# Kernel tuning notes

Measured on AMD Instinct MI355X. Metric: run time of the kernel, lower is better.

## Reference

```python
import jax, jax.numpy as jnp
import numpy as np

B, S = 128, 32
V, E, H, L = 32000, 512, 1024, 2


def setup_inputs() -> dict:
    key = jax.random.key(0)
    ks = jax.random.split(key, 16)
    s = 0.02  # weight scale
    inp = {
        "x": jax.random.randint(ks[0], (B, S), 0, V),
        "encoder_output": jax.random.normal(ks[1], (S, B, H), jnp.float32),  # unused by module
        "encoder_hidden_state": jax.random.normal(ks[2], (L, B, H), jnp.float32),
        "emb": jax.random.normal(ks[3], (V, E), jnp.float32) * s,
        "w_ih0": jax.random.normal(ks[4], (3 * H, E), jnp.float32) * s,
        "w_hh0": jax.random.normal(ks[5], (3 * H, H), jnp.float32) * s,
        "b_ih0": jax.random.normal(ks[6], (3 * H,), jnp.float32) * s,
        "b_hh0": jax.random.normal(ks[7], (3 * H,), jnp.float32) * s,
        "w_ih1": jax.random.normal(ks[8], (3 * H, H), jnp.float32) * s,
        "w_hh1": jax.random.normal(ks[9], (3 * H, H), jnp.float32) * s,
        "b_ih1": jax.random.normal(ks[10], (3 * H,), jnp.float32) * s,
        "b_hh1": jax.random.normal(ks[11], (3 * H,), jnp.float32) * s,
        "w_dec": jax.random.normal(ks[12], (V, H), jnp.float32) * s,
        "b_dec": jax.random.normal(ks[13], (V,), jnp.float32) * s,
        "max_seq_length": S,
    }
    return inp


def _gru_cell(h, xt, w_ih, w_hh, b_ih, b_hh):
    # PyTorch GRU gate math
    gi = xt @ w_ih.T + b_ih  # [B, 3H]
    gh = h @ w_hh.T + b_hh   # [B, 3H]
    ir, iz, inn = jnp.split(gi, 3, axis=-1)
    hr, hz, hn = jnp.split(gh, 3, axis=-1)
    r = jax.nn.sigmoid(ir + hr)
    z = jax.nn.sigmoid(iz + hz)
    n = jnp.tanh(inn + r * hn)
    return (1.0 - z) * n + z * h


def reference(x, encoder_output, encoder_hidden_state, emb,
              w_ih0, w_hh0, b_ih0, b_hh0,
              w_ih1, w_hh1, b_ih1, b_hh1,
              w_dec, b_dec, max_seq_length):
    # teaching_rate = 0.0 -> pure teacher forcing; dropout p=0.0 -> identity.
    # Step 0 consumes SOS token (id 1, from torch.ones().long()); steps 1..T-1 consume x[:, i].
    Bsz = x.shape[0]
    sos = jnp.ones((Bsz, 1), jnp.int32)
    toks = jnp.concatenate([sos, x[:, 1:max_seq_length].astype(jnp.int32)], axis=1)  # [B, T]
    xs = emb[toks].transpose(1, 0, 2)  # [T, B, E] (seq-first, matching permute(1,0,2))

    def step(carry, xt):
        h0, h1 = carry
        h0 = _gru_cell(h0, xt, w_ih0, w_hh0, b_ih0, b_hh0)
        h1 = _gru_cell(h1, h0, w_ih1, w_hh1, b_ih1, b_hh1)
        return (h0, h1), h1

    init = (encoder_hidden_state[0], encoder_hidden_state[1])
    _, ys = jax.lax.scan(step, init, xs)  # ys: [T, B, H]
    logits = jnp.einsum('tbh,vh->tbv', ys, w_dec) + b_dec  # [T, B, V]
    return logits
```

## Files before the change

### kernel.cpp

```cpp
#include <hip/hip_runtime.h>
#include <hip/hip_bf16.h>
#include <stdint.h>

#define T_SEQ 32
#define BATCH 128
#define EMB   512
#define HID   1024
#define VOC   32000
#define G3    (3 * HID)
#define MROWS (T_SEQ * BATCH)
#define BHID  (BATCH * HID)

typedef __bf16 bf16_t;
typedef __bf16 bf16x8 __attribute__((ext_vector_type(8)));
typedef __bf16 bf16x4 __attribute__((ext_vector_type(4)));
typedef float  f32x4  __attribute__((ext_vector_type(4)));

#define MFMA(a, b, c) __builtin_amdgcn_mfma_f32_16x16x32_bf16((a), (b), (c), 0, 0, 0)

__global__ void f32_to_bf16_kernel(const float* __restrict__ in,
                                   bf16_t* __restrict__ out, int n) {
    int i = (blockIdx.x * blockDim.x + threadIdx.x) * 4;
    if (i + 3 < n) {
        float4 v = *(const float4*)(in + i);
        out[i + 0] = (bf16_t)v.x;
        out[i + 1] = (bf16_t)v.y;
        out[i + 2] = (bf16_t)v.z;
        out[i + 3] = (bf16_t)v.w;
    } else {
        for (; i < n; ++i) out[i] = (bf16_t)in[i];
    }
}

__global__ void embed_kernel(const int* __restrict__ x,
                             const float* __restrict__ emb,
                             bf16_t* __restrict__ X) {
    int m = blockIdx.x;
    int t = m >> 7, b = m & 127;
    int tok = (t == 0) ? 1 : x[b * T_SEQ + t];
    const float* src = emb + (size_t)tok * EMB;
    bf16_t* dst = X + (size_t)m * EMB;
    int c = threadIdx.x * 4;
    float4 v = *(const float4*)(src + c);
    dst[c + 0] = (bf16_t)v.x;
    dst[c + 1] = (bf16_t)v.y;
    dst[c + 2] = (bf16_t)v.z;
    dst[c + 3] = (bf16_t)v.w;
}

#define GLOAD_LDS16(g, l)                                                    \
    __builtin_amdgcn_global_load_lds(                                        \
        (const __attribute__((address_space(1))) void*)(g),                  \
        (__attribute__((address_space(3))) void*)(l), 16, 0, 0)

template <int BIAS>
__global__ __launch_bounds__(256) void gemm_bf16_kernel(
    const bf16_t* __restrict__ A, const bf16_t* __restrict__ B,
    const float* __restrict__ bias, float* __restrict__ C,
    int M, int N, int K) {
    __shared__ __align__(16) bf16_t As[128 * 32];
    __shared__ __align__(16) bf16_t Bs[128 * 32];

    const int nbm = gridDim.y, nbn = gridDim.x;
    const int nwg = nbm * nbn;
    int lin = blockIdx.y * nbn + blockIdx.x;
    if ((nwg & 7) == 0) {
        int xcd = lin & 7, idx = lin >> 3;
        lin = xcd * (nwg >> 3) + idx;
    }
    const int bm = (lin % nbm) * 128;
    const int bn = (lin / nbm) * 128;

    const int tid  = threadIdx.x;
    const int lane = tid & 63;
    const int w    = tid >> 6;
    const int wr   = w >> 1, wc = w & 1;

    f32x4 acc[4][4] = {};

    const int lrow = tid >> 2;
    const int lcol = (tid & 3) * 8;
    const bf16_t* ag = A + (size_t)(bm + lrow) * K + lcol;
    const bf16_t* bg = B + (size_t)(bn + lrow) * K + lcol;
    bf16_t* asl0 = As + lrow * 32 + lcol;
    bf16_t* asl1 = As + (lrow + 64) * 32 + lcol;
    bf16_t* bsl0 = Bs + lrow * 32 + lcol;
    bf16_t* bsl1 = Bs + (lrow + 64) * 32 + lcol;

    const int r16 = lane & 15;
    const int kh  = (lane >> 4) * 8;

    for (int k0 = 0; k0 < K; k0 += 32) {
        GLOAD_LDS16(ag + k0, asl0);
        GLOAD_LDS16(ag + (size_t)64 * K + k0, asl1);
        GLOAD_LDS16(bg + k0, bsl0);
        GLOAD_LDS16(bg + (size_t)64 * K + k0, bsl1);
        __syncthreads();

        bf16x8 af[4], bf[4];
#pragma unroll
        for (int mi = 0; mi < 4; ++mi)
            af[mi] = *(const bf16x8*)(As + (wr * 64 + mi * 16 + r16) * 32 + kh);
#pragma unroll
        for (int ni = 0; ni < 4; ++ni)
            bf[ni] = *(const bf16x8*)(Bs + (wc * 64 + ni * 16 + r16) * 32 + kh);
#pragma unroll
        for (int mi = 0; mi < 4; ++mi)
#pragma unroll
            for (int ni = 0; ni < 4; ++ni)
                acc[mi][ni] = MFMA(af[mi], bf[ni], acc[mi][ni]);
        __syncthreads();
    }

#pragma unroll
    for (int mi = 0; mi < 4; ++mi) {
        const int row0 = bm + wr * 64 + mi * 16 + (lane >> 4) * 4;
#pragma unroll
        for (int ni = 0; ni < 4; ++ni) {
            const int col = bn + wc * 64 + ni * 16 + r16;
            float bv = 0.f;
            if (BIAS) bv = bias[col];
#pragma unroll
            for (int r = 0; r < 4; ++r)
                C[(size_t)(row0 + r) * N + col] = acc[mi][ni][r] + bv;
        }
    }
}

template <int BIAS>
__global__ __launch_bounds__(512, 1) void gemm256_bf16_kernel(
    const bf16_t* __restrict__ A, const bf16_t* __restrict__ B,
    const float* __restrict__ bias, float* __restrict__ C,
    int M, int N, int K) {
    __shared__ __align__(16) bf16_t lds[2 * 2 * 16384];

    const int NT = K >> 6;
    const int nbm = gridDim.y, nbn = gridDim.x;
    const int nwg = nbm * nbn;
    int lin = blockIdx.y * nbn + blockIdx.x;
    {
        int q = nwg >> 3, r = nwg & 7, x = lin & 7, i = lin >> 3;
        lin = (x < r ? x * (q + 1) : r * (q + 1) + (x - r) * q) + i;
    }
    const int bm = (lin % nbm) * 256;
    const int bn = (lin / nbm) * 256;

    const int tid = threadIdx.x, lane = tid & 63;
    const int w = tid >> 6, wm = w >> 2, wn = w & 3;
    const int r16 = lane & 15, sl = lane >> 4, r7 = r16 & 7;

    const int srow  = tid >> 3;
    const int sslot = (tid & 7) ^ (srow & 7);
    const bf16_t* agS = A + (size_t)(bm + srow) * K + sslot * 8;
    const bf16_t* bgS = B + (size_t)(bn + srow) * K + sslot * 8;

    const int colk0 = ((0 + sl) ^ r7) * 8;
    const int colk1 = ((4 + sl) ^ r7) * 8;
    const int arow = (wm * 128 + r16) * 64;
    const int brow = (wn * 64 + r16) * 64;

    f32x4 acc[8][4] = {};
    bf16x8 af[4][2], bf[4][2];

#pragma unroll
    for (int l = 0; l < 4; ++l)
        GLOAD_LDS16(agS + (size_t)(l * 64) * K, lds + l * 4096 + tid * 8);
#pragma unroll
    for (int l = 0; l < 4; ++l)
        GLOAD_LDS16(bgS + (size_t)(l * 64) * K, lds + 16384 + l * 4096 + tid * 8);
#pragma unroll
    for (int l = 0; l < 4; ++l)
        GLOAD_LDS16(agS + (size_t)(l * 64) * K + 64,
                    lds + 32768 + l * 4096 + tid * 8);
#pragma unroll
    for (int l = 0; l < 4; ++l)
        GLOAD_LDS16(bgS + (size_t)(l * 64) * K + 64,
                    lds + 49152 + l * 4096 + tid * 8);
    asm volatile("s_waitcnt vmcnt(8)" ::: "memory");
    __builtin_amdgcn_sched_barrier(0);
    __builtin_amdgcn_s_barrier();

#pragma unroll 1
    for (int kt = 0; kt < NT; ++kt) {
        const int cur = kt & 1;
        const bf16_t* Ab = lds + cur * 32768;
        const bf16_t* Bb = Ab + 16384;
        bf16_t* Sb = lds + cur * 32768;
        const bool st = (kt + 2 < NT);
        const size_t kof = (size_t)(kt + 2) * 64;

#pragma unroll
        for (int fr = 0; fr < 4; ++fr) {
            af[fr][0] = *(const bf16x8*)(Ab + arow + fr * 1024 + colk0);
            af[fr][1] = *(const bf16x8*)(Ab + arow + fr * 1024 + colk1);
        }
#pragma unroll
        for (int nf = 0; nf < 2; ++nf) {
            bf[nf][0] = *(const bf16x8*)(Bb + brow + nf * 1024 + colk0);
            bf[nf][1] = *(const bf16x8*)(Bb + brow + nf * 1024 + colk1);
        }
        __builtin_amdgcn_sched_barrier(0);
        __builtin_amdgcn_s_barrier();
        asm volatile("s_waitcnt lgkmcnt(0)" ::: "memory");
        __builtin_amdgcn_sched_barrier(0);
        __builtin_amdgcn_s_setprio(1);
#pragma unroll
        for (int fr = 0; fr < 4; ++fr)
#pragma unroll
            for (int nf = 0; nf < 2; ++nf) {
                acc[fr][nf] = MFMA(af[fr][0], bf[nf][0], acc[fr][nf]);
                acc[fr][nf] = MFMA(af[fr][1], bf[nf][1], acc[fr][nf]);
            }
        __builtin_amdgcn_s_setprio(0);
        __builtin_amdgcn_sched_barrier(0);
        __builtin_amdgcn_s_barrier();

#pragma unroll
        for (int nf = 2; nf < 4; ++nf) {
            bf[nf][0] = *(const bf16x8*)(Bb + brow + nf * 1024 + colk0);
            bf[nf][1] = *(const bf16x8*)(Bb + brow + nf * 1024 + colk1);
        }
        __builtin_amdgcn_sched_barrier(0);
        if (st) {
            GLOAD_LDS16(agS + kof, Sb + tid * 8);
            GLOAD_LDS16(agS + (size_t)128 * K + kof, Sb + 8192 + tid * 8);
        }
        __builtin_amdgcn_s_barrier();
        asm volatile("s_waitcnt lgkmcnt(0)" ::: "memory");
        __builtin_amdgcn_sched_barrier(0);
        __builtin_amdgcn_s_setprio(1);
#pragma unroll
        for (int fr = 0; fr < 4; ++fr)
#pragma unroll
            for (int nf = 2; nf < 4; ++nf) {
                acc[fr][nf] = MFMA(af[fr][0], bf[nf][0], acc[fr][nf]);
                acc[fr][nf] = MFMA(af[fr][1], bf[nf][1], acc[fr][nf]);
            }
        __builtin_amdgcn_s_setprio(0);
        __builtin_amdgcn_sched_barrier(0);
        __builtin_amdgcn_s_barrier();

#pragma unroll
        for (int fr = 0; fr < 4; ++fr) {
            af[fr][0] = *(const bf16x8*)(Ab + arow + (fr + 4) * 1024 + colk0);
            af[fr][1] = *(const bf16x8*)(Ab + arow + (fr + 4) * 1024 + colk1);
        }
        __builtin_amdgcn_sched_barrier(0);
        if (st) {
#pragma unroll
            for (int l = 0; l < 4; ++l)
                GLOAD_LDS16(bgS + (size_t)(l * 64) * K + kof,
                            Sb + 16384 + l * 4096 + tid * 8);
        }
        __builtin_amdgcn_s_barrier();
        asm volatile("s_waitcnt lgkmcnt(0)" ::: "memory");
        __builtin_amdgcn_sched_barrier(0);
        __builtin_amdgcn_s_setprio(1);
#pragma unroll
        for (int fr = 0; fr < 4; ++fr)
#pragma unroll
            for (int nf = 0; nf < 2; ++nf) {
                acc[fr + 4][nf] = MFMA(af[fr][0], bf[nf][0], acc[fr + 4][nf]);
                acc[fr + 4][nf] = MFMA(af[fr][1], bf[nf][1], acc[fr + 4][nf]);
            }
        __builtin_amdgcn_s_setprio(0);
        __builtin_amdgcn_sched_barrier(0);
        __builtin_amdgcn_s_barrier();

        if (st) {
            GLOAD_LDS16(agS + (size_t)64 * K + kof, Sb + 4096 + tid * 8);
            GLOAD_LDS16(agS + (size_t)192 * K + kof, Sb + 12288 + tid * 8);
        }
        if (kt + 2 < NT) {
            asm volatile("s_waitcnt vmcnt(8)" ::: "memory");
        } else if (kt + 1 < NT) {
            asm volatile("s_waitcnt vmcnt(0)" ::: "memory");
        }
        __builtin_amdgcn_sched_barrier(0);
        __builtin_amdgcn_s_setprio(1);
#pragma unroll
        for (int fr = 0; fr < 4; ++fr)
#pragma unroll
            for (int nf = 2; nf < 4; ++nf) {
                acc[fr + 4][nf] = MFMA(af[fr][0], bf[nf][0], acc[fr + 4][nf]);
                acc[fr + 4][nf] = MFMA(af[fr][1], bf[nf][1], acc[fr + 4][nf]);
            }
        __builtin_amdgcn_s_setprio(0);
        __builtin_amdgcn_sched_barrier(0);
        __builtin_amdgcn_s_barrier();
    }

#pragma unroll
    for (int fr = 0; fr < 8; ++fr) {
        const int row0 = bm + wm * 128 + fr * 16 + sl * 4;
#pragma unroll
        for (int nf = 0; nf < 4; ++nf) {
            const int col = bn + wn * 64 + nf * 16 + r16;
            float bv = 0.f;
            if (BIAS) bv = bias[col];
#pragma unroll
            for (int r = 0; r < 4; ++r)
                __builtin_nontemporal_store(
                    acc[fr][nf][r] + bv, &C[(size_t)(row0 + r) * N + col]);
        }
    }
}

union U64cast  { bf16x4 v; unsigned long long u; };
union U128cast { f32x4 v; unsigned long long u[2]; };

__device__ __forceinline__ unsigned flag_ld(const unsigned* p) {
    return __hip_atomic_load(p, __ATOMIC_RELAXED, __HIP_MEMORY_SCOPE_SYSTEM);
}
__device__ __forceinline__ void flag_st(unsigned* p, unsigned v) {
    __hip_atomic_store(p, v, __ATOMIC_RELAXED, __HIP_MEMORY_SCOPE_SYSTEM);
}

__global__ __launch_bounds__(256, 1) void fused_scan_kernel(
    const bf16_t* __restrict__ h0ib, const bf16_t* __restrict__ h1ib,
    const float* __restrict__ enc_hid,
    const bf16_t* __restrict__ whh0, const bf16_t* __restrict__ wih1,
    const bf16_t* __restrict__ whh1,
    const float* __restrict__ bhh0, const float* __restrict__ bih1,
    const float* __restrict__ bhh1,
    float* __restrict__ Gi, bf16_t* __restrict__ H0b,
    bf16_t* __restrict__ H1b, unsigned* __restrict__ flags) {
    __shared__ __align__(16) float Sg[4][3][128][16];

    const int tid  = threadIdx.x;
    const int lane = tid & 63;
    const int w    = tid >> 6;
    const int role = blockIdx.x >> 6;
    const int cb   = blockIdx.x & 63;
    const int c0   = cb * 16;
    const int r16  = lane & 15;
    const int kq   = (lane >> 4) * 8;
    const int pf   = w * 16 + (lane & 15);

    const bf16_t* whh = role == 0 ? whh0 : (role == 1 ? wih1 : whh1);
    const float*  bia = role == 0 ? bhh0 : (role == 1 ? bih1 : bhh1);

    bf16x8 wf[3][8];
#pragma unroll
    for (int g = 0; g < 3; ++g)
#pragma unroll
        for (int kf = 0; kf < 8; ++kf)
            wf[g][kf] = *(const bf16x8*)(
                whh + (size_t)(g * HID + c0 + r16) * HID + w * 256 + kf * 32 + kq);

    const int cg   = tid & 3;
    const int rloc = tid >> 2;
    const int ce   = c0 + cg * 4;

    float bh[3][4];
#pragma unroll
    for (int g = 0; g < 3; ++g)
#pragma unroll
        for (int j = 0; j < 4; ++j) bh[g][j] = bia[g * HID + ce + j];

    float hp[2][4];
    if (role != 1) {
        const float* h0f = enc_hid + (role == 2 ? BHID : 0);
#pragma unroll
        for (int i = 0; i < 2; ++i)
#pragma unroll
            for (int j = 0; j < 4; ++j)
                hp[i][j] = h0f[(size_t)(rloc + i * 64) * HID + ce + j];
    }

    for (int t = 0; t < T_SEQ; ++t) {
        if (role == 0) {
            if (t)
                while (flag_ld(&flags[pf]) < (unsigned)t)
                    __builtin_amdgcn_s_sleep(1);
        } else if (role == 1) {
            while (flag_ld(&flags[pf]) < (unsigned)(t + 1))
                __builtin_amdgcn_s_sleep(1);
        } else {
            if (t)
                while (flag_ld(&flags[128 + pf]) < (unsigned)t)
                    __builtin_amdgcn_s_sleep(1);
        }

        f32x4 gi[2][3];
        if (role == 0) {
#pragma unroll
            for (int i = 0; i < 2; ++i) {
                const size_t gb =
                    ((size_t)t * BATCH + rloc + i * 64) * G3 + ce;
                gi[i][0] = *(const f32x4*)(Gi + gb);
                gi[i][1] = *(const f32x4*)(Gi + gb + HID);
                gi[i][2] = *(const f32x4*)(Gi + gb + 2 * HID);
            }
        }

        const bf16_t* hb =
            role == 0 ? (t ? H0b + (size_t)(t - 1) * BHID : h0ib)
          : role == 1 ? (H0b + (size_t)t * BHID)
                      : (t ? H1b + (size_t)(t - 1) * BHID : h1ib);

        f32x4 acc[3][8] = {};
        bf16x8 af[4][8];
#define LD_GROUP(buf, kf)                                                    \
    {                                                                        \
        const int kbase = w * 256 + (kf) * 32 + kq;                          \
        _Pragma("unroll") for (int rf = 0; rf < 8; ++rf)                     \
            af[buf][rf] =                                                    \
                *(const bf16x8*)(hb + (size_t)(rf * 16 + r16) * HID + kbase); \
    }
        LD_GROUP(0, 0)
        LD_GROUP(1, 1)
        LD_GROUP(2, 2)
#pragma unroll
        for (int kf = 0; kf < 8; ++kf) {
            if (kf + 3 < 8) LD_GROUP((kf + 3) & 3, kf + 3)
#pragma unroll
            for (int rf = 0; rf < 8; ++rf) {
                acc[0][rf] = MFMA(af[kf & 3][rf], wf[0][kf], acc[0][rf]);
                acc[1][rf] = MFMA(af[kf & 3][rf], wf[1][kf], acc[1][rf]);
                acc[2][rf] = MFMA(af[kf & 3][rf], wf[2][kf], acc[2][rf]);
            }
        }
#undef LD_GROUP

#pragma unroll
        for (int g = 0; g < 3; ++g)
#pragma unroll
            for (int rf = 0; rf < 8; ++rf)
#pragma unroll
                for (int r = 0; r < 4; ++r)
                    Sg[w][g][rf * 16 + (lane >> 4) * 4 + r][r16] = acc[g][rf][r];
        __syncthreads();

        if (role == 2) {
            while (flag_ld(&flags[64 + cb]) < (unsigned)(t + 1))
                __builtin_amdgcn_s_sleep(1);
#pragma unroll
            for (int i = 0; i < 2; ++i) {
                const size_t gb =
                    ((size_t)t * BATCH + rloc + i * 64) * G3 + ce;
#pragma unroll
                for (int g = 0; g < 3; ++g) {
                    U128cast u;
                    const unsigned long long* p =
                        (const unsigned long long*)(Gi + gb + g * HID);
                    u.u[0] = __hip_atomic_load(p, __ATOMIC_RELAXED,
                                               __HIP_MEMORY_SCOPE_SYSTEM);
                    u.u[1] = __hip_atomic_load(p + 1, __ATOMIC_RELAXED,
                                               __HIP_MEMORY_SCOPE_SYSTEM);
                    gi[i][g] = u.v;
                }
            }
        }

#pragma unroll
        for (int i = 0; i < 2; ++i) {
            const int row = rloc + i * 64;
            f32x4 gr = *(const f32x4*)&Sg[0][0][row][cg * 4];
            f32x4 gz = *(const f32x4*)&Sg[0][1][row][cg * 4];
            f32x4 gn = *(const f32x4*)&Sg[0][2][row][cg * 4];
#pragma unroll
            for (int ks = 1; ks < 4; ++ks) {
                gr += *(const f32x4*)&Sg[ks][0][row][cg * 4];
                gz += *(const f32x4*)&Sg[ks][1][row][cg * 4];
                gn += *(const f32x4*)&Sg[ks][2][row][cg * 4];
            }
            if (role == 1) {
                const size_t gb =
                    ((size_t)t * BATCH + row) * G3 + ce;
                U128cast s0, s1, s2;
#pragma unroll
                for (int j = 0; j < 4; ++j) {
                    s0.v[j] = gr[j] + bh[0][j];
                    s1.v[j] = gz[j] + bh[1][j];
                    s2.v[j] = gn[j] + bh[2][j];
                }
                unsigned long long* p0 = (unsigned long long*)(Gi + gb);
                unsigned long long* p1 = (unsigned long long*)(Gi + gb + HID);
                unsigned long long* p2 = (unsigned long long*)(Gi + gb + 2 * HID);
                __hip_atomic_store(p0, s0.u[0], __ATOMIC_RELAXED, __HIP_MEMORY_SCOPE_SYSTEM);
                __hip_atomic_store(p0 + 1, s0.u[1], __ATOMIC_RELAXED, __HIP_MEMORY_SCOPE_SYSTEM);
                __hip_atomic_store(p1, s1.u[0], __ATOMIC_RELAXED, __HIP_MEMORY_SCOPE_SYSTEM);
                __hip_atomic_store(p1 + 1, s1.u[1], __ATOMIC_RELAXED, __HIP_MEMORY_SCOPE_SYSTEM);
                __hip_atomic_store(p2, s2.u[0], __ATOMIC_RELAXED, __HIP_MEMORY_SCOPE_SYSTEM);
                __hip_atomic_store(p2 + 1, s2.u[1], __ATOMIC_RELAXED, __HIP_MEMORY_SCOPE_SYSTEM);
            } else {
                U64cast hb4;
#pragma unroll
                for (int j = 0; j < 4; ++j) {
                    float rr = 1.f / (1.f + __expf(-(gi[i][0][j] + gr[j] + bh[0][j])));
                    float zz = 1.f / (1.f + __expf(-(gi[i][1][j] + gz[j] + bh[1][j])));
                    float nn = tanhf(gi[i][2][j] + rr * (gn[j] + bh[2][j]));
                    float h  = (1.f - zz) * nn + zz * hp[i][j];
                    hp[i][j] = h;
                    hb4.v[j] = (bf16_t)h;
                }
                bf16_t* dst = (role == 0 ? H0b : H1b) +
                              (size_t)t * BHID + (size_t)row * HID + ce;
                __hip_atomic_store((unsigned long long*)dst, hb4.u,
                                   __ATOMIC_RELAXED, __HIP_MEMORY_SCOPE_SYSTEM);
            }
        }

        __syncthreads();
        if (tid == 0)
            flag_st(&flags[role * 64 + cb], (unsigned)(t + 1));
    }
}

extern "C" void kernel_launch(void* const* d_in, const int* in_sizes, int n_in,
                              void* d_out, int out_size, void* d_ws, size_t ws_size,
                              hipStream_t stream) {
    const int*   x        = (const int*)d_in[0];
    const float* enc_hid  = (const float*)d_in[2];
    const float* emb      = (const float*)d_in[3];
    const float* w_ih0    = (const float*)d_in[4];
    const float* w_hh0    = (const float*)d_in[5];
    const float* b_ih0    = (const float*)d_in[6];
    const float* b_hh0    = (const float*)d_in[7];
    const float* w_ih1    = (const float*)d_in[8];
    const float* w_hh1    = (const float*)d_in[9];
    const float* b_ih1    = (const float*)d_in[10];
    const float* b_hh1    = (const float*)d_in[11];
    const float* w_dec    = (const float*)d_in[12];
    const float* b_dec    = (const float*)d_in[13];
    float* out = (float*)d_out;

    char* ws = (char*)d_ws;
    size_t off = 0;
    auto alloc = [&](size_t bytes) {
        void* p = ws + off;
        off += (bytes + 255) & ~(size_t)255;
        return p;
    };
    unsigned* flags  = (unsigned*)alloc(1024);
    bf16_t* Xb     = (bf16_t*)alloc((size_t)MROWS * EMB * 2);
    bf16_t* Wih0b  = (bf16_t*)alloc((size_t)G3 * EMB * 2);
    bf16_t* Whh0b  = (bf16_t*)alloc((size_t)G3 * HID * 2);
    bf16_t* Wih1b  = (bf16_t*)alloc((size_t)G3 * HID * 2);
    bf16_t* Whh1b  = (bf16_t*)alloc((size_t)G3 * HID * 2);
    bf16_t* Wdecb  = (bf16_t*)alloc((size_t)VOC * HID * 2);
    bf16_t* h0ib   = (bf16_t*)alloc((size_t)BATCH * HID * 2);
    bf16_t* h1ib   = (bf16_t*)alloc((size_t)BATCH * HID * 2);
    float*  Gi     = (float*)alloc((size_t)MROWS * G3 * 4);
    bf16_t* H0b    = (bf16_t*)alloc((size_t)MROWS * HID * 2);
    bf16_t* H1b    = (bf16_t*)alloc((size_t)MROWS * HID * 2);

    hipMemsetAsync(flags, 0, 1024, stream);

    auto cvt = [&](const float* src, bf16_t* dst, int n) {
        int blocks = (n + 1023) / 1024;
        f32_to_bf16_kernel<<<blocks, 256, 0, stream>>>(src, dst, n);
    };

    cvt(w_ih0, Wih0b, G3 * EMB);
    cvt(w_hh0, Whh0b, G3 * HID);
    cvt(w_ih1, Wih1b, G3 * HID);
    cvt(w_hh1, Whh1b, G3 * HID);
    cvt(w_dec, Wdecb, VOC * HID);
    cvt(enc_hid, h0ib, BATCH * HID);
    cvt(enc_hid + BATCH * HID, h1ib, BATCH * HID);

    embed_kernel<<<MROWS, 128, 0, stream>>>(x, emb, Xb);

    gemm_bf16_kernel<1><<<dim3(G3 / 128, MROWS / 128), 256, 0, stream>>>(
        Xb, Wih0b, b_ih0, Gi, MROWS, G3, EMB);

    fused_scan_kernel<<<192, 256, 0, stream>>>(
        h0ib, h1ib, enc_hid, Whh0b, Wih1b, Whh1b,
        b_hh0, b_ih1, b_hh1, Gi, H0b, H1b, flags);

    gemm256_bf16_kernel<1><<<dim3(VOC / 256, MROWS / 256), 512, 0, stream>>>(
        H1b, Wdecb, b_dec, out, MROWS, VOC, HID);
}
```

Baseline: 966.6 us.

## Use per-wave flags in scan kernel, prefetch Gi, fuse weight conversions

Each wave now publishes its own completion flag right after its global stores drain, so consumers wait on finer-grained flags instead of one flag per block set after a trailing barrier. The layer-1 hh role checks the Gi-ready flags before its GEMM, and the layer-0 role prefetches the next step's Gi while the barrier is pending. The seven f32-to-bf16 conversion launches are merged into one kernel to cut launch overhead. The finer flags add more polling traffic, and correctness depends on the explicit vmcnt wait ordering the stores before each flag.

```diff
diff --git a/kernel.cpp b/kernel.cpp
--- a/kernel.cpp
+++ b/kernel.cpp
@@ -18,18 +18,41 @@
 
 #define MFMA(a, b, c) __builtin_amdgcn_mfma_f32_16x16x32_bf16((a), (b), (c), 0, 0, 0)
 
-__global__ void f32_to_bf16_kernel(const float* __restrict__ in,
-                                   bf16_t* __restrict__ out, int n) {
-    int i = (blockIdx.x * blockDim.x + threadIdx.x) * 4;
-    if (i + 3 < n) {
-        float4 v = *(const float4*)(in + i);
-        out[i + 0] = (bf16_t)v.x;
-        out[i + 1] = (bf16_t)v.y;
-        out[i + 2] = (bf16_t)v.z;
-        out[i + 3] = (bf16_t)v.w;
-    } else {
-        for (; i < n; ++i) out[i] = (bf16_t)in[i];
-    }
+union U64cast  { bf16x4 v; unsigned long long u; };
+union U128cast { f32x4 v; unsigned long long u[2]; };
+
+__device__ __forceinline__ unsigned flag_ld(const unsigned* p) {
+    return __hip_atomic_load(p, __ATOMIC_RELAXED, __HIP_MEMORY_SCOPE_SYSTEM);
+}
+__device__ __forceinline__ void flag_st(unsigned* p, unsigned v) {
+    __hip_atomic_store(p, v, __ATOMIC_RELAXED, __HIP_MEMORY_SCOPE_SYSTEM);
+}
+
+__global__ void fused_cvt_kernel(
+    const float* __restrict__ w_ih0, const float* __restrict__ w_hh0,
+    const float* __restrict__ w_ih1, const float* __restrict__ w_hh1,
+    const float* __restrict__ w_dec, const float* __restrict__ enc_hid,
+    bf16_t* __restrict__ Wih0b, bf16_t* __restrict__ Whh0b,
+    bf16_t* __restrict__ Wih1b, bf16_t* __restrict__ Whh1b,
+    bf16_t* __restrict__ Wdecb, bf16_t* __restrict__ h0ib,
+    bf16_t* __restrict__ h1ib) {
+    const int b = blockIdx.x;
+    const float* src;
+    bf16_t* dst;
+    int base;
+    if (b < 1536)       { src = w_ih0;          dst = Wih0b; base = b; }
+    else if (b < 4608)  { src = w_hh0;          dst = Whh0b; base = b - 1536; }
+    else if (b < 7680)  { src = w_ih1;          dst = Wih1b; base = b - 4608; }
+    else if (b < 10752) { src = w_hh1;          dst = Whh1b; base = b - 7680; }
+    else if (b < 42752) { src = w_dec;          dst = Wdecb; base = b - 10752; }
+    else if (b < 42880) { src = enc_hid;        dst = h0ib;  base = b - 42752; }
+    else                { src = enc_hid + BHID; dst = h1ib;  base = b - 42880; }
+    const int i = base * 1024 + threadIdx.x * 4;
+    float4 v = *(const float4*)(src + i);
+    dst[i + 0] = (bf16_t)v.x;
+    dst[i + 1] = (bf16_t)v.y;
+    dst[i + 2] = (bf16_t)v.z;
+    dst[i + 3] = (bf16_t)v.w;
 }
 
 __global__ void embed_kernel(const int* __restrict__ x,
@@ -306,16 +329,6 @@
     }
 }
 
-union U64cast  { bf16x4 v; unsigned long long u; };
-union U128cast { f32x4 v; unsigned long long u[2]; };
-
-__device__ __forceinline__ unsigned flag_ld(const unsigned* p) {
-    return __hip_atomic_load(p, __ATOMIC_RELAXED, __HIP_MEMORY_SCOPE_SYSTEM);
-}
-__device__ __forceinline__ void flag_st(unsigned* p, unsigned v) {
-    __hip_atomic_store(p, v, __ATOMIC_RELAXED, __HIP_MEMORY_SCOPE_SYSTEM);
-}
-
 __global__ __launch_bounds__(256, 1) void fused_scan_kernel(
     const bf16_t* __restrict__ h0ib, const bf16_t* __restrict__ h1ib,
     const float* __restrict__ enc_hid,
@@ -324,7 +337,7 @@
     const float* __restrict__ bhh0, const float* __restrict__ bih1,
     const float* __restrict__ bhh1,
     float* __restrict__ Gi, bf16_t* __restrict__ H0b,
-    bf16_t* __restrict__ H1b, unsigned* __restrict__ flags) {
+    bf16_t* __restrict__ H1b, unsigned* __restrict__ wfl) {
     __shared__ __align__(16) float Sg[4][3][128][16];
 
     const int tid  = threadIdx.x;
@@ -335,7 +348,8 @@
     const int c0   = cb * 16;
     const int r16  = lane & 15;
     const int kq   = (lane >> 4) * 8;
-    const int pf   = w * 16 + (lane & 15);
+
+    const int FL0 = 0, FG = 256, FL1 = 512;
 
     const bf16_t* whh = role == 0 ? whh0 : (role == 1 ? wih1 : whh1);
     const float*  bia = role == 0 ? bhh0 : (role == 1 ? bih1 : bhh1);
@@ -368,73 +382,49 @@
                 hp[i][j] = h0f[(size_t)(rloc + i * 64) * HID + ce + j];
     }
 
+    f32x4 gi[2][3];
+    if (role == 0) {
+#pragma unroll
+        for (int i = 0; i < 2; ++i) {
+            const size_t gb = (size_t)(rloc + i * 64) * G3 + ce;
+            gi[i][0] = *(const f32x4*)(Gi + gb);
+            gi[i][1] = *(const f32x4*)(Gi + gb + HID);
+            gi[i][2] = *(const f32x4*)(Gi + gb + 2 * HID);
+        }
+    }
+
     for (int t = 0; t < T_SEQ; ++t) {
         if (role == 0) {
-            if (t)
-                while (flag_ld(&flags[pf]) < (unsigned)t)
+            if (t && tid < 64) {
+#pragma unroll
+                for (int j = 0; j < 4; ++j)
+                    while (flag_ld(&wfl[FL0 + tid * 4 + j]) < (unsigned)t)
+                        __builtin_amdgcn_s_sleep(1);
+            }
+        } else if (role == 1) {
+            if (tid < 64) {
+#pragma unroll
+                for (int j = 0; j < 4; ++j)
+                    while (flag_ld(&wfl[FL0 + tid * 4 + j]) < (unsigned)(t + 1))
+                        __builtin_amdgcn_s_sleep(1);
+            }
+        } else {
+            if (tid < 64) {
+                if (t) {
+#pragma unroll
+                    for (int j = 0; j < 4; ++j)
+                        while (flag_ld(&wfl[FL1 + tid * 4 + j]) < (unsigned)t)
+                            __builtin_amdgcn_s_sleep(1);
+                }
+            } else if (tid < 68) {
+                while (flag_ld(&wfl[FG + cb * 4 + (tid - 64)]) <
+                       (unsigned)(t + 1))
                     __builtin_amdgcn_s_sleep(1);
-        } else if (role == 1) {
-            while (flag_ld(&flags[pf]) < (unsigned)(t + 1))
-                __builtin_amdgcn_s_sleep(1);
-        } else {
-            if (t)
-                while (flag_ld(&flags[128 + pf]) < (unsigned)t)
-                    __builtin_amdgcn_s_sleep(1);
-        }
-
-        f32x4 gi[2][3];
-        if (role == 0) {
-#pragma unroll
-            for (int i = 0; i < 2; ++i) {
-                const size_t gb =
-                    ((size_t)t * BATCH + rloc + i * 64) * G3 + ce;
-                gi[i][0] = *(const f32x4*)(Gi + gb);
-                gi[i][1] = *(const f32x4*)(Gi + gb + HID);
-                gi[i][2] = *(const f32x4*)(Gi + gb + 2 * HID);
-            }
-        }
-
-        const bf16_t* hb =
-            role == 0 ? (t ? H0b + (size_t)(t - 1) * BHID : h0ib)
-          : role == 1 ? (H0b + (size_t)t * BHID)
-                      : (t ? H1b + (size_t)(t - 1) * BHID : h1ib);
-
-        f32x4 acc[3][8] = {};
-        bf16x8 af[4][8];
-#define LD_GROUP(buf, kf)                                                    \
-    {                                                                        \
-        const int kbase = w * 256 + (kf) * 32 + kq;                          \
-        _Pragma("unroll") for (int rf = 0; rf < 8; ++rf)                     \
-            af[buf][rf] =                                                    \
-                *(const bf16x8*)(hb + (size_t)(rf * 16 + r16) * HID + kbase); \
-    }
-        LD_GROUP(0, 0)
-        LD_GROUP(1, 1)
-        LD_GROUP(2, 2)
-#pragma unroll
-        for (int kf = 0; kf < 8; ++kf) {
-            if (kf + 3 < 8) LD_GROUP((kf + 3) & 3, kf + 3)
-#pragma unroll
-            for (int rf = 0; rf < 8; ++rf) {
-                acc[0][rf] = MFMA(af[kf & 3][rf], wf[0][kf], acc[0][rf]);
-                acc[1][rf] = MFMA(af[kf & 3][rf], wf[1][kf], acc[1][rf]);
-                acc[2][rf] = MFMA(af[kf & 3][rf], wf[2][kf], acc[2][rf]);
-            }
-        }
-#undef LD_GROUP
-
-#pragma unroll
-        for (int g = 0; g < 3; ++g)
-#pragma unroll
-            for (int rf = 0; rf < 8; ++rf)
-#pragma unroll
-                for (int r = 0; r < 4; ++r)
-                    Sg[w][g][rf * 16 + (lane >> 4) * 4 + r][r16] = acc[g][rf][r];
+            }
+        }
         __syncthreads();
 
         if (role == 2) {
-            while (flag_ld(&flags[64 + cb]) < (unsigned)(t + 1))
-                __builtin_amdgcn_s_sleep(1);
 #pragma unroll
             for (int i = 0; i < 2; ++i) {
                 const size_t gb =
@@ -453,6 +443,44 @@
             }
         }
 
+        const bf16_t* hb =
+            role == 0 ? (t ? H0b + (size_t)(t - 1) * BHID : h0ib)
+          : role == 1 ? (H0b + (size_t)t * BHID)
+                      : (t ? H1b + (size_t)(t - 1) * BHID : h1ib);
+
+        f32x4 acc[3][8] = {};
+        bf16x8 af[4][8];
+#define LD_GROUP(buf, kf)                                                    \
+    {                                                                        \
+        const int kbase = w * 256 + (kf) * 32 + kq;                          \
+        _Pragma("unroll") for (int rf = 0; rf < 8; ++rf)                     \
+            af[buf][rf] =                                                    \
+                *(const bf16x8*)(hb + (size_t)(rf * 16 + r16) * HID + kbase); \
+    }
+        LD_GROUP(0, 0)
+        LD_GROUP(1, 1)
+        LD_GROUP(2, 2)
+#pragma unroll
+        for (int kf = 0; kf < 8; ++kf) {
+            if (kf + 3 < 8) LD_GROUP((kf + 3) & 3, kf + 3)
+#pragma unroll
+            for (int rf = 0; rf < 8; ++rf) {
+                acc[0][rf] = MFMA(af[kf & 3][rf], wf[0][kf], acc[0][rf]);
+                acc[1][rf] = MFMA(af[kf & 3][rf], wf[1][kf], acc[1][rf]);
+                acc[2][rf] = MFMA(af[kf & 3][rf], wf[2][kf], acc[2][rf]);
+            }
+        }
+#undef LD_GROUP
+
+#pragma unroll
+        for (int g = 0; g < 3; ++g)
+#pragma unroll
+            for (int rf = 0; rf < 8; ++rf)
+#pragma unroll
+                for (int r = 0; r < 4; ++r)
+                    Sg[w][g][rf * 16 + (lane >> 4) * 4 + r][r16] = acc[g][rf][r];
+        __syncthreads();
+
 #pragma unroll
         for (int i = 0; i < 2; ++i) {
             const int row = rloc + i * 64;
@@ -466,8 +494,7 @@
                 gn += *(const f32x4*)&Sg[ks][2][row][cg * 4];
             }
             if (role == 1) {
-                const size_t gb =
-                    ((size_t)t * BATCH + row) * G3 + ce;
+                const size_t gb = ((size_t)t * BATCH + row) * G3 + ce;
                 U128cast s0, s1, s2;
 #pragma unroll
                 for (int j = 0; j < 4; ++j) {
@@ -502,9 +529,22 @@
             }
         }
 
+        asm volatile("s_waitcnt vmcnt(0)" ::: "memory");
+        __builtin_amdgcn_sched_barrier(0);
+        if (lane == 0)
+            flag_st(&wfl[role * 256 + cb * 4 + w], (unsigned)(t + 1));
+
+        if (role == 0 && t + 1 < T_SEQ) {
+#pragma unroll
+            for (int i = 0; i < 2; ++i) {
+                const size_t gb =
+                    ((size_t)(t + 1) * BATCH + rloc + i * 64) * G3 + ce;
+                gi[i][0] = *(const f32x4*)(Gi + gb);
+                gi[i][1] = *(const f32x4*)(Gi + gb + HID);
+                gi[i][2] = *(const f32x4*)(Gi + gb + 2 * HID);
+            }
+        }
         __syncthreads();
-        if (tid == 0)
-            flag_st(&flags[role * 64 + cb], (unsigned)(t + 1));
     }
 }
 
@@ -533,7 +573,7 @@
         off += (bytes + 255) & ~(size_t)255;
         return p;
     };
-    unsigned* flags  = (unsigned*)alloc(1024);
+    unsigned* wfl  = (unsigned*)alloc(4096);
     bf16_t* Xb     = (bf16_t*)alloc((size_t)MROWS * EMB * 2);
     bf16_t* Wih0b  = (bf16_t*)alloc((size_t)G3 * EMB * 2);
     bf16_t* Whh0b  = (bf16_t*)alloc((size_t)G3 * HID * 2);
@@ -546,20 +586,11 @@
     bf16_t* H0b    = (bf16_t*)alloc((size_t)MROWS * HID * 2);
     bf16_t* H1b    = (bf16_t*)alloc((size_t)MROWS * HID * 2);
 
-    hipMemsetAsync(flags, 0, 1024, stream);
-
-    auto cvt = [&](const float* src, bf16_t* dst, int n) {
-        int blocks = (n + 1023) / 1024;
-        f32_to_bf16_kernel<<<blocks, 256, 0, stream>>>(src, dst, n);
-    };
-
-    cvt(w_ih0, Wih0b, G3 * EMB);
-    cvt(w_hh0, Whh0b, G3 * HID);
-    cvt(w_ih1, Wih1b, G3 * HID);
-    cvt(w_hh1, Whh1b, G3 * HID);
-    cvt(w_dec, Wdecb, VOC * HID);
-    cvt(enc_hid, h0ib, BATCH * HID);
-    cvt(enc_hid + BATCH * HID, h1ib, BATCH * HID);
+    hipMemsetAsync(wfl, 0, 4096, stream);
+
+    fused_cvt_kernel<<<43008, 256, 0, stream>>>(
+        w_ih0, w_hh0, w_ih1, w_hh1, w_dec, enc_hid,
+        Wih0b, Whh0b, Wih1b, Whh1b, Wdecb, h0ib, h1ib);
 
     embed_kernel<<<MROWS, 128, 0, stream>>>(x, emb, Xb);
 
@@ -568,7 +599,7 @@
 
     fused_scan_kernel<<<192, 256, 0, stream>>>(
         h0ib, h1ib, enc_hid, Whh0b, Wih1b, Whh1b,
-        b_hh0, b_ih1, b_hh1, Gi, H0b, H1b, flags);
+        b_hh0, b_ih1, b_hh1, Gi, H0b, H1b, wfl);
 
     gemm256_bf16_kernel<1><<<dim3(VOC / 256, MROWS / 256), 512, 0, stream>>>(
         H1b, Wdecb, b_dec, out, MROWS, VOC, HID);
```

After: 906.7 us. 1.07x faster.
